# Performance work log

Measured on AMD Instinct MI355X. Metric: run time of the kernel, lower is better.

## Reference

```python
import jax, jax.numpy as jnp
import numpy as np

M1, M2 = 20, 20  # retained DCT modes per layer

def dct1_last(x):
    # scipy.fftpack unnormalized DCT-I along last axis via FFT of even extension
    N = x.shape[-1]
    ext = jnp.concatenate([x, x[..., -2:0:-1]], axis=-1)  # length 2N-2
    return jnp.fft.rfft(ext).real[..., :N]

def dct1_2d(x):
    x = dct1_last(x)                       # along axis -1
    x = dct1_last(x.swapaxes(-1, -2)).swapaxes(-1, -2)  # along axis -2
    return x

def setup_inputs() -> dict:
    key = jax.random.key(0)
    ks = jax.random.split(key, 11)
    B, X, Y, Din, C, FC, Dout, L = 8, 256, 256, 3, 64, 128, 1, 3
    scale = 1.0 / (C * C)
    return {
        "x": jax.random.normal(ks[0], (B, X, Y, Din), jnp.float32),
        "fc0_w": jax.random.normal(ks[1], (Din, C), jnp.float32) * 0.1,
        "fc0_b": jax.random.normal(ks[2], (C,), jnp.float32) * 0.1,
        "sp_w1": scale * jax.random.uniform(ks[3], (L, C, C, M1, M2), jnp.float32),
        "sp_w2": scale * jax.random.uniform(ks[4], (L, C, C, M1, M2), jnp.float32),
        "conv_w": jax.random.normal(ks[5], (L, C, C), jnp.float32) * 0.05,
        "conv_b": jax.random.normal(ks[6], (L, C), jnp.float32) * 0.05,
        "fc1_w": jax.random.normal(ks[7], (C, FC), jnp.float32) * 0.05,
        "fc1_b": jax.random.normal(ks[8], (FC,), jnp.float32) * 0.05,
        "fc2_w": jax.random.normal(ks[9], (FC, Dout), jnp.float32) * 0.05,
        "fc2_b": jax.random.normal(ks[10], (Dout,), jnp.float32) * 0.05,
    }

def reference(x, fc0_w, fc0_b, sp_w1, sp_w2, conv_w, conv_b, fc1_w, fc1_b, fc2_w, fc2_b):
    h = x @ fc0_w + fc0_b                  # (B, X, Y, C)
    h = h.transpose(0, 3, 1, 2)            # (B, C, X, Y)
    B, C, X, Y = h.shape
    n_layers = sp_w1.shape[0]
    for i in range(n_layers):
        hd = dct1_2d(h)                    # forward DCT-I (unnormalized)
        # spectral mode multiply, scattered into zero spectrum (imag part is 0)
        out = jnp.zeros((B, C, X, Y), h.dtype)
        out = out.at[:, :, :M1, :M2].set(
            jnp.einsum('bixy,ioxy->boxy', hd[:, :, :M1, :M2], sp_w1[i]))
        out = out.at[:, :, X - M1:, :M2].set(
            jnp.einsum('bixy,ioxy->boxy', hd[:, :, X - M1:, :M2], sp_w2[i]))
        x1 = dct1_2d(out)                  # fftpack idct type-1 == dct type-1 (unnormalized)
        x2 = jnp.einsum('bixy,oi->boxy', h, conv_w[i]) + conv_b[i][None, :, None, None]
        h = x1 + x2
        if i != n_layers - 1:
            h = jnp.tanh(h)
    h = h.transpose(0, 2, 3, 1)            # (B, X, Y, C)
    h = jnp.tanh(h @ fc1_w + fc1_b)
    return h @ fc2_w + fc2_b               # (B, X, Y, 1)
```

## Files before the change

### kernel.cpp

```cpp
#include <hip/hip_runtime.h>
#include <math.h>

#define BB    8
#define CC    64
#define NN    256
#define MM    20
#define NKK   40
#define NLAY  3
#define FCD   128
#define PLANE (NN*NN)

__device__ __forceinline__ float fast_tanh(float x) {
    float xc = fminf(fmaxf(x, -15.f), 15.f);
    float e = __expf(2.f * xc);
    return (e - 1.f) / (e + 1.f);
}

__global__ __launch_bounds__(256) void k_basis(float* __restrict__ FlT, float* __restrict__ FkT,
                                               float* __restrict__ BkT, float* __restrict__ BlT,
                                               float* __restrict__ CwT, const float* __restrict__ conv_w) {
    int t = threadIdx.x;
    const double PI = 3.14159265358979323846;
    for (int j = t; j < NN*MM; j += 256) {
        int y = j / MM, l = j % MM;
        double g = (y == 0 || y == NN-1) ? 1.0 : 2.0;
        FlT[j] = (float)(g * cos(PI * (double)(l*y) / (double)(NN-1)));
    }
    for (int j = t; j < NN*NKK; j += 256) {
        int x = j / NKK, k = j % NKK;
        int rk = (k < MM) ? k : (NN - NKK + k);
        double g = (x == 0 || x == NN-1) ? 1.0 : 2.0;
        FkT[j] = (float)(g * cos(PI * (double)(rk*x) / (double)(NN-1)));
    }
    for (int j = t; j < NKK*NN; j += 256) {
        int k = j / NN, p = j % NN;
        int rk = (k < MM) ? k : (NN - NKK + k);
        double g = (rk == 0 || rk == NN-1) ? 1.0 : 2.0;
        BkT[j] = (float)(g * cos(PI * (double)(rk*p) / (double)(NN-1)));
    }
    for (int j = t; j < MM*NN; j += 256) {
        int l = j / NN, q = j % NN;
        double g = (l == 0) ? 1.0 : 2.0;
        BlT[j] = (float)(g * cos(PI * (double)(q*l) / (double)(NN-1)));
    }
    for (int j = t; j < NLAY*CC*CC; j += 256) {
        int lay = j / (CC*CC), r = j % (CC*CC);
        int i = r / CC, o = r % CC;
        CwT[j] = conv_w[lay*CC*CC + o*CC + i];
    }
}

__global__ __launch_bounds__(256) void k_fc0(const float* __restrict__ xin, const float* __restrict__ w,
                                             const float* __restrict__ bias, float* __restrict__ h) {
    __shared__ float xs[NN*3];
    int b = blockIdx.x >> 8, p = blockIdx.x & 255, q = threadIdx.x;
    size_t rowbase = ((size_t)(b*NN + p)*NN) * 3;
    for (int j = q; j < NN*3; j += 256) xs[j] = xin[rowbase + j];
    __syncthreads();
    float v0 = xs[q*3+0], v1 = xs[q*3+1], v2 = xs[q*3+2];
    size_t obase = (size_t)b*CC*PLANE + (size_t)p*NN + q;
    #pragma unroll 8
    for (int c = 0; c < CC; ++c) {
        float hv = bias[c] + v0*w[c] + v1*w[CC+c] + v2*w[2*CC+c];
        h[obase + (size_t)c*PLANE] = hv;
    }
}

__global__ __launch_bounds__(256, 2) void k_fwd(const float* __restrict__ h, const float* __restrict__ FkT,
                                                const float* __restrict__ FlT, float* __restrict__ Gt) {
    __shared__ float P[NKK][NN+1];
    int plane = blockIdx.x;
    int t = threadIdx.x;
    const float* hp = h + (size_t)plane * PLANE;
    float acc[NKK];
    #pragma unroll 40
    for (int k = 0; k < NKK; ++k) acc[k] = 0.f;
    #pragma unroll 2
    for (int x = 0; x < NN; ++x) {
        float hv = hp[x*NN + t];
        const float* fr = &FkT[x*NKK];
        #pragma unroll 40
        for (int k = 0; k < NKK; ++k) acc[k] += fr[k] * hv;
    }
    #pragma unroll 40
    for (int k = 0; k < NKK; ++k) P[k][t] = acc[k];
    __syncthreads();
    int b = plane >> 6, c = plane & 63;
    for (int j = t; j < NKK*MM; j += 256) {
        int k = j / MM, l = j % MM;
        float a = 0.f;
        for (int y = 0; y < NN; ++y) a += P[k][y] * FlT[y*MM + l];
        Gt[((size_t)(k*BB + b)*CC + c)*MM + l] = a;
    }
}

__global__ __launch_bounds__(256, 2) void k_spec(const float* __restrict__ Gt, const float* __restrict__ w1,
                                                 const float* __restrict__ w2, float* __restrict__ S) {
    extern __shared__ float gl[];
    int kb = blockIdx.x;
    int t = threadIdx.x;
    const float* chunk = Gt + (size_t)kb * (BB*CC*MM);
    for (int j = t; j < BB*CC*MM; j += 256) gl[j] = chunk[j];
    __syncthreads();
    int o = t & 63, g = t >> 6;
    int b0 = 2*g, b1 = 2*g + 1;
    const float* wp; int kk;
    if (kb < MM) { wp = w1; kk = kb; } else { wp = w2; kk = kb - MM; }
    float a0[MM], a1[MM];
    #pragma unroll 20
    for (int l = 0; l < MM; ++l) { a0[l] = 0.f; a1[l] = 0.f; }
    for (int i = 0; i < CC; ++i) {
        const float4* wr4 = reinterpret_cast<const float4*>(wp + ((size_t)(i*CC + o)*MM + kk)*MM);
        const float4* g04 = reinterpret_cast<const float4*>(&gl[(b0*CC + i)*MM]);
        const float4* g14 = reinterpret_cast<const float4*>(&gl[(b1*CC + i)*MM]);
        #pragma unroll 5
        for (int l4 = 0; l4 < MM/4; ++l4) {
            float4 wv = wr4[l4];
            float4 gv0 = g04[l4];
            float4 gv1 = g14[l4];
            a0[4*l4+0] += wv.x*gv0.x; a0[4*l4+1] += wv.y*gv0.y;
            a0[4*l4+2] += wv.z*gv0.z; a0[4*l4+3] += wv.w*gv0.w;
            a1[4*l4+0] += wv.x*gv1.x; a1[4*l4+1] += wv.y*gv1.y;
            a1[4*l4+2] += wv.z*gv1.z; a1[4*l4+3] += wv.w*gv1.w;
        }
    }
    #pragma unroll 20
    for (int l = 0; l < MM; ++l) {
        S[((size_t)(b0*NKK + kb)*MM + l)*CC + o] = a0[l];
        S[((size_t)(b1*NKK + kb)*MM + l)*CC + o] = a1[l];
    }
}

__global__ __launch_bounds__(256, 2) void k_inv1(const float* __restrict__ S, const float* __restrict__ BkT,
                                                 float* __restrict__ U) {
    int b = blockIdx.x >> 8, p = blockIdx.x & 255;
    int o = threadIdx.x & 63, w = threadIdx.x >> 6;
    float acc[5];
    #pragma unroll 5
    for (int j = 0; j < 5; ++j) acc[j] = 0.f;
    for (int k = 0; k < NKK; ++k) {
        float bk = BkT[k*NN + p];
        const float* sb = S + ((size_t)(b*NKK + k)*MM + w)*CC + o;
        #pragma unroll 5
        for (int j = 0; j < 5; ++j) acc[j] += bk * sb[(size_t)(4*j)*CC];
    }
    float* ub = U + ((size_t)(b*NN + p)*MM + w)*CC + o;
    #pragma unroll 5
    for (int j = 0; j < 5; ++j) ub[(size_t)(4*j)*CC] = acc[j];
}

__global__ __launch_bounds__(256, 2) void k_combine(float* h, const float* __restrict__ U,
                                                    const float* __restrict__ BlT, const float* __restrict__ cwt,
                                                    const float* __restrict__ cb) {
    int b = blockIdx.x >> 8, p = blockIdx.x & 255;
    int q = threadIdx.x;
    float acc[CC];
    #pragma unroll 64
    for (int o = 0; o < CC; ++o) acc[o] = cb[o];
    float* hb = h + (size_t)b*CC*PLANE + (size_t)p*NN + q;
    #pragma unroll 4
    for (int i = 0; i < CC; ++i) {
        float hv = hb[(size_t)i*PLANE];
        const float* wr = &cwt[i*CC];
        #pragma unroll 64
        for (int o = 0; o < CC; ++o) acc[o] += wr[o]*hv;
    }
    const float* ub = U + ((size_t)(b*NN + p)*MM)*CC;
    #pragma unroll 2
    for (int l = 0; l < MM; ++l) {
        float blv = BlT[l*NN + q];
        const float* ur = ub + (size_t)l*CC;
        #pragma unroll 64
        for (int o = 0; o < CC; ++o) acc[o] += ur[o]*blv;
    }
    #pragma unroll 64
    for (int o = 0; o < CC; ++o) hb[(size_t)o*PLANE] = fast_tanh(acc[o]);
}

__global__ __launch_bounds__(256, 2) void k_combine_fc(const float* __restrict__ h, const float* __restrict__ U,
        const float* __restrict__ BlT, const float* __restrict__ cwt, const float* __restrict__ cb,
        const float* __restrict__ w1, const float* __restrict__ b1,
        const float* __restrict__ w2, const float* __restrict__ b2, float* __restrict__ out) {
    int b = blockIdx.x >> 8, p = blockIdx.x & 255;
    int q = threadIdx.x;
    float acc[CC];
    #pragma unroll 64
    for (int o = 0; o < CC; ++o) acc[o] = cb[o];
    const float* hb = h + (size_t)b*CC*PLANE + (size_t)p*NN + q;
    #pragma unroll 4
    for (int i = 0; i < CC; ++i) {
        float hv = hb[(size_t)i*PLANE];
        const float* wr = &cwt[i*CC];
        #pragma unroll 64
        for (int o = 0; o < CC; ++o) acc[o] += wr[o]*hv;
    }
    const float* ub = U + ((size_t)(b*NN + p)*MM)*CC;
    #pragma unroll 2
    for (int l = 0; l < MM; ++l) {
        float blv = BlT[l*NN + q];
        const float* ur = ub + (size_t)l*CC;
        #pragma unroll 64
        for (int o = 0; o < CC; ++o) acc[o] += ur[o]*blv;
    }
    float ov = b2[0];
    const int FCH = 8;
    for (int f0 = 0; f0 < FCD; f0 += FCH) {
        float a[FCH];
        #pragma unroll 8
        for (int f = 0; f < FCH; ++f) a[f] = b1[f0 + f];
        #pragma unroll 64
        for (int i = 0; i < CC; ++i) {
            float hv = acc[i];
            const float* wr = &w1[i*FCD + f0];
            #pragma unroll 8
            for (int f = 0; f < FCH; ++f) a[f] += hv*wr[f];
        }
        #pragma unroll 8
        for (int f = 0; f < FCH; ++f) ov += fast_tanh(a[f]) * w2[f0 + f];
    }
    out[(size_t)blockIdx.x*NN + q] = ov;
}

extern "C" void kernel_launch(void* const* d_in, const int* in_sizes, int n_in,
                              void* d_out, int out_size, void* d_ws, size_t ws_size,
                              hipStream_t stream) {
    const float* x      = (const float*)d_in[0];
    const float* fc0_w  = (const float*)d_in[1];
    const float* fc0_b  = (const float*)d_in[2];
    const float* sp_w1  = (const float*)d_in[3];
    const float* sp_w2  = (const float*)d_in[4];
    const float* conv_w = (const float*)d_in[5];
    const float* conv_b = (const float*)d_in[6];
    const float* fc1_w  = (const float*)d_in[7];
    const float* fc1_b  = (const float*)d_in[8];
    const float* fc2_w  = (const float*)d_in[9];
    const float* fc2_b  = (const float*)d_in[10];

    float* ws = (float*)d_ws;
    const size_t HSZ = (size_t)BB*CC*PLANE;
    float* hA  = ws;
    float* Gt  = hA + HSZ;
    float* S   = Gt + (size_t)NKK*BB*CC*MM;
    float* U   = S  + (size_t)BB*NKK*MM*CC;
    float* FlT = U  + (size_t)BB*NN*MM*CC;
    float* FkT = FlT + NN*MM;
    float* BkT = FkT + NN*NKK;
    float* BlT = BkT + NKK*NN;
    float* CwT = BlT + MM*NN;

    k_basis<<<1, 256, 0, stream>>>(FlT, FkT, BkT, BlT, CwT, conv_w);
    k_fc0<<<BB*NN, 256, 0, stream>>>(x, fc0_w, fc0_b, hA);

    for (int lay = 0; lay < NLAY; ++lay) {
        const float* w1 = sp_w1 + (size_t)lay*CC*CC*MM*MM;
        const float* w2 = sp_w2 + (size_t)lay*CC*CC*MM*MM;
        k_fwd<<<BB*CC, 256, 0, stream>>>(hA, FkT, FlT, Gt);
        k_spec<<<NKK, 256, BB*CC*MM*sizeof(float), stream>>>(Gt, w1, w2, S);
        k_inv1<<<BB*NN, 256, 0, stream>>>(S, BkT, U);
        if (lay != NLAY-1) {
            k_combine<<<BB*NN, 256, 0, stream>>>(
                hA, U, BlT, CwT + lay*CC*CC, conv_b + lay*CC);
        } else {
            k_combine_fc<<<BB*NN, 256, 0, stream>>>(
                hA, U, BlT, CwT + lay*CC*CC, conv_b + lay*CC,
                fc1_w, fc1_b, fc2_w, fc2_b, (float*)d_out);
        }
    }
}
```

Baseline: 1.060 ms.

## Split combine kernels across output-channel groups per wavefront to cut register pressure

Each combine block now covers 64 spatial columns, and its four wavefronts each own 16 output channels instead of one thread owning all 64 channels. This lowers per-thread accumulators from 64 to 16 to raise occupancy, at the price of four times as many blocks and each h element being loaded by four wavefronts. The in-place combine adds a __syncthreads before writing, so every wavefront has read h before any wavefront overwrites it. The final-layer kernel stages the 64-channel activation in shared memory, splits the FC1 hidden units across wavefronts, and reduces the partial outputs through shared memory.

```diff
diff --git a/kernel.cpp b/kernel.cpp
--- a/kernel.cpp
+++ b/kernel.cpp
@@ -152,73 +152,97 @@
 __global__ __launch_bounds__(256, 2) void k_combine(float* h, const float* __restrict__ U,
                                                     const float* __restrict__ BlT, const float* __restrict__ cwt,
                                                     const float* __restrict__ cb) {
-    int b = blockIdx.x >> 8, p = blockIdx.x & 255;
-    int q = threadIdx.x;
-    float acc[CC];
-    #pragma unroll 64
-    for (int o = 0; o < CC; ++o) acc[o] = cb[o];
+    int b = blockIdx.x >> 10, rem = blockIdx.x & 1023;
+    int p = rem >> 2, qc = rem & 3;
+    int lane = threadIdx.x & 63, w = threadIdx.x >> 6;
+    int q = qc*64 + lane, ob = w*16;
+    float acc[16];
+    {
+        const float* cbw = &cb[ob];
+        #pragma unroll 16
+        for (int o = 0; o < 16; ++o) acc[o] = cbw[o];
+    }
     float* hb = h + (size_t)b*CC*PLANE + (size_t)p*NN + q;
     #pragma unroll 4
     for (int i = 0; i < CC; ++i) {
         float hv = hb[(size_t)i*PLANE];
-        const float* wr = &cwt[i*CC];
-        #pragma unroll 64
-        for (int o = 0; o < CC; ++o) acc[o] += wr[o]*hv;
-    }
-    const float* ub = U + ((size_t)(b*NN + p)*MM)*CC;
-    #pragma unroll 2
+        const float* wr = &cwt[i*CC + ob];
+        #pragma unroll 16
+        for (int o = 0; o < 16; ++o) acc[o] += wr[o]*hv;
+    }
+    const float* ub = U + ((size_t)(b*NN + p)*MM)*CC + ob;
+    #pragma unroll 4
     for (int l = 0; l < MM; ++l) {
         float blv = BlT[l*NN + q];
         const float* ur = ub + (size_t)l*CC;
-        #pragma unroll 64
-        for (int o = 0; o < CC; ++o) acc[o] += ur[o]*blv;
-    }
-    #pragma unroll 64
-    for (int o = 0; o < CC; ++o) hb[(size_t)o*PLANE] = fast_tanh(acc[o]);
+        #pragma unroll 16
+        for (int o = 0; o < 16; ++o) acc[o] += ur[o]*blv;
+    }
+    __syncthreads();
+    #pragma unroll 16
+    for (int o = 0; o < 16; ++o) hb[(size_t)(ob + o)*PLANE] = fast_tanh(acc[o]);
 }
 
 __global__ __launch_bounds__(256, 2) void k_combine_fc(const float* __restrict__ h, const float* __restrict__ U,
         const float* __restrict__ BlT, const float* __restrict__ cwt, const float* __restrict__ cb,
         const float* __restrict__ w1, const float* __restrict__ b1,
         const float* __restrict__ w2, const float* __restrict__ b2, float* __restrict__ out) {
-    int b = blockIdx.x >> 8, p = blockIdx.x & 255;
-    int q = threadIdx.x;
-    float acc[CC];
-    #pragma unroll 64
-    for (int o = 0; o < CC; ++o) acc[o] = cb[o];
+    __shared__ float tile[CC][65];
+    __shared__ float part[4][64];
+    int b = blockIdx.x >> 10, rem = blockIdx.x & 1023;
+    int p = rem >> 2, qc = rem & 3;
+    int lane = threadIdx.x & 63, w = threadIdx.x >> 6;
+    int q = qc*64 + lane, ob = w*16;
+    float acc[16];
+    {
+        const float* cbw = &cb[ob];
+        #pragma unroll 16
+        for (int o = 0; o < 16; ++o) acc[o] = cbw[o];
+    }
     const float* hb = h + (size_t)b*CC*PLANE + (size_t)p*NN + q;
     #pragma unroll 4
     for (int i = 0; i < CC; ++i) {
         float hv = hb[(size_t)i*PLANE];
-        const float* wr = &cwt[i*CC];
-        #pragma unroll 64
-        for (int o = 0; o < CC; ++o) acc[o] += wr[o]*hv;
-    }
-    const float* ub = U + ((size_t)(b*NN + p)*MM)*CC;
-    #pragma unroll 2
+        const float* wr = &cwt[i*CC + ob];
+        #pragma unroll 16
+        for (int o = 0; o < 16; ++o) acc[o] += wr[o]*hv;
+    }
+    const float* ub = U + ((size_t)(b*NN + p)*MM)*CC + ob;
+    #pragma unroll 4
     for (int l = 0; l < MM; ++l) {
         float blv = BlT[l*NN + q];
         const float* ur = ub + (size_t)l*CC;
-        #pragma unroll 64
-        for (int o = 0; o < CC; ++o) acc[o] += ur[o]*blv;
-    }
-    float ov = b2[0];
-    const int FCH = 8;
-    for (int f0 = 0; f0 < FCD; f0 += FCH) {
-        float a[FCH];
-        #pragma unroll 8
-        for (int f = 0; f < FCH; ++f) a[f] = b1[f0 + f];
-        #pragma unroll 64
-        for (int i = 0; i < CC; ++i) {
-            float hv = acc[i];
-            const float* wr = &w1[i*FCD + f0];
-            #pragma unroll 8
-            for (int f = 0; f < FCH; ++f) a[f] += hv*wr[f];
-        }
-        #pragma unroll 8
-        for (int f = 0; f < FCH; ++f) ov += fast_tanh(a[f]) * w2[f0 + f];
-    }
-    out[(size_t)blockIdx.x*NN + q] = ov;
+        #pragma unroll 16
+        for (int o = 0; o < 16; ++o) acc[o] += ur[o]*blv;
+    }
+    #pragma unroll 16
+    for (int o = 0; o < 16; ++o) tile[ob + o][lane] = acc[o];
+    __syncthreads();
+    float a[32];
+    {
+        const float* bw = &b1[w*32];
+        #pragma unroll 32
+        for (int f = 0; f < 32; ++f) a[f] = bw[f];
+    }
+    #pragma unroll 2
+    for (int i = 0; i < CC; ++i) {
+        float hv = tile[i][lane];
+        const float* wr = &w1[i*FCD + w*32];
+        #pragma unroll 32
+        for (int f = 0; f < 32; ++f) a[f] += hv*wr[f];
+    }
+    float ov = 0.f;
+    {
+        const float* w2w = &w2[w*32];
+        #pragma unroll 32
+        for (int f = 0; f < 32; ++f) ov += fast_tanh(a[f]) * w2w[f];
+    }
+    part[w][lane] = ov;
+    __syncthreads();
+    if (threadIdx.x < 64) {
+        float r = b2[0] + part[0][lane] + part[1][lane] + part[2][lane] + part[3][lane];
+        out[((size_t)(b*NN + p)*NN) + qc*64 + lane] = r;
+    }
 }
 
 extern "C" void kernel_launch(void* const* d_in, const int* in_sizes, int n_in,
@@ -258,10 +282,10 @@
         k_spec<<<NKK, 256, BB*CC*MM*sizeof(float), stream>>>(Gt, w1, w2, S);
         k_inv1<<<BB*NN, 256, 0, stream>>>(S, BkT, U);
         if (lay != NLAY-1) {
-            k_combine<<<BB*NN, 256, 0, stream>>>(
+            k_combine<<<BB*NN*4, 256, 0, stream>>>(
                 hA, U, BlT, CwT + lay*CC*CC, conv_b + lay*CC);
         } else {
-            k_combine_fc<<<BB*NN, 256, 0, stream>>>(
+            k_combine_fc<<<BB*NN*4, 256, 0, stream>>>(
                 hA, U, BlT, CwT + lay*CC*CC, conv_b + lay*CC,
                 fc1_w, fc1_b, fc2_w, fc2_b, (float*)d_out);
         }
```

New measurement: 2.095 ms. 1.98x slower.

## Stage h column in LDS and compute combine outputs in 8-channel chunks

Applied to the files above, without the earlier changes.

The combine kernels now load the 64-channel input column into a 64KB shared tile and loop over output channels in groups of 8, instead of holding 64 accumulators in registers. The final kernel also writes the pre-activation back to global memory and reloads it into the tile for the FC layers. The aim is to cut register pressure and spilling. In exchange it adds 64KB of LDS per block, which caps occupancy, plus extra global round-trips and eight passes over the weights.

```diff
diff --git a/kernel.cpp b/kernel.cpp
--- a/kernel.cpp
+++ b/kernel.cpp
@@ -152,71 +152,96 @@
 __global__ __launch_bounds__(256, 2) void k_combine(float* h, const float* __restrict__ U,
                                                     const float* __restrict__ BlT, const float* __restrict__ cwt,
                                                     const float* __restrict__ cb) {
+    __shared__ float tile[CC][NN];
     int b = blockIdx.x >> 8, p = blockIdx.x & 255;
     int q = threadIdx.x;
-    float acc[CC];
-    #pragma unroll 64
-    for (int o = 0; o < CC; ++o) acc[o] = cb[o];
     float* hb = h + (size_t)b*CC*PLANE + (size_t)p*NN + q;
-    #pragma unroll 4
-    for (int i = 0; i < CC; ++i) {
-        float hv = hb[(size_t)i*PLANE];
-        const float* wr = &cwt[i*CC];
-        #pragma unroll 64
-        for (int o = 0; o < CC; ++o) acc[o] += wr[o]*hv;
-    }
+    #pragma unroll 8
+    for (int i = 0; i < CC; ++i) tile[i][q] = hb[(size_t)i*PLANE];
+    float blv[MM];
+    #pragma unroll 20
+    for (int l = 0; l < MM; ++l) blv[l] = BlT[l*NN + q];
     const float* ub = U + ((size_t)(b*NN + p)*MM)*CC;
-    #pragma unroll 2
-    for (int l = 0; l < MM; ++l) {
-        float blv = BlT[l*NN + q];
-        const float* ur = ub + (size_t)l*CC;
-        #pragma unroll 64
-        for (int o = 0; o < CC; ++o) acc[o] += ur[o]*blv;
-    }
-    #pragma unroll 64
-    for (int o = 0; o < CC; ++o) hb[(size_t)o*PLANE] = fast_tanh(acc[o]);
-}
-
-__global__ __launch_bounds__(256, 2) void k_combine_fc(const float* __restrict__ h, const float* __restrict__ U,
+    __syncthreads();
+    for (int oc = 0; oc < CC/8; ++oc) {
+        float acc8[8];
+        const float* cbw = &cb[oc*8];
+        #pragma unroll 8
+        for (int f = 0; f < 8; ++f) acc8[f] = cbw[f];
+        #pragma unroll 4
+        for (int i = 0; i < CC; ++i) {
+            float hv = tile[i][q];
+            const float* wr = &cwt[i*CC + oc*8];
+            #pragma unroll 8
+            for (int f = 0; f < 8; ++f) acc8[f] += wr[f]*hv;
+        }
+        #pragma unroll 4
+        for (int l = 0; l < MM; ++l) {
+            const float* ur = ub + (size_t)l*CC + oc*8;
+            #pragma unroll 8
+            for (int f = 0; f < 8; ++f) acc8[f] += ur[f]*blv[l];
+        }
+        #pragma unroll 8
+        for (int f = 0; f < 8; ++f) hb[(size_t)(oc*8+f)*PLANE] = fast_tanh(acc8[f]);
+    }
+}
+
+__global__ __launch_bounds__(256, 2) void k_combine_fc(float* h, const float* __restrict__ U,
         const float* __restrict__ BlT, const float* __restrict__ cwt, const float* __restrict__ cb,
         const float* __restrict__ w1, const float* __restrict__ b1,
         const float* __restrict__ w2, const float* __restrict__ b2, float* __restrict__ out) {
+    __shared__ float tile[CC][NN];
     int b = blockIdx.x >> 8, p = blockIdx.x & 255;
     int q = threadIdx.x;
-    float acc[CC];
-    #pragma unroll 64
-    for (int o = 0; o < CC; ++o) acc[o] = cb[o];
-    const float* hb = h + (size_t)b*CC*PLANE + (size_t)p*NN + q;
-    #pragma unroll 4
-    for (int i = 0; i < CC; ++i) {
-        float hv = hb[(size_t)i*PLANE];
-        const float* wr = &cwt[i*CC];
-        #pragma unroll 64
-        for (int o = 0; o < CC; ++o) acc[o] += wr[o]*hv;
-    }
+    float* hb = h + (size_t)b*CC*PLANE + (size_t)p*NN + q;
+    #pragma unroll 8
+    for (int i = 0; i < CC; ++i) tile[i][q] = hb[(size_t)i*PLANE];
+    float blv[MM];
+    #pragma unroll 20
+    for (int l = 0; l < MM; ++l) blv[l] = BlT[l*NN + q];
     const float* ub = U + ((size_t)(b*NN + p)*MM)*CC;
-    #pragma unroll 2
-    for (int l = 0; l < MM; ++l) {
-        float blv = BlT[l*NN + q];
-        const float* ur = ub + (size_t)l*CC;
-        #pragma unroll 64
-        for (int o = 0; o < CC; ++o) acc[o] += ur[o]*blv;
-    }
+    __syncthreads();
+    for (int oc = 0; oc < CC/8; ++oc) {
+        float acc8[8];
+        const float* cbw = &cb[oc*8];
+        #pragma unroll 8
+        for (int f = 0; f < 8; ++f) acc8[f] = cbw[f];
+        #pragma unroll 4
+        for (int i = 0; i < CC; ++i) {
+            float hv = tile[i][q];
+            const float* wr = &cwt[i*CC + oc*8];
+            #pragma unroll 8
+            for (int f = 0; f < 8; ++f) acc8[f] += wr[f]*hv;
+        }
+        #pragma unroll 4
+        for (int l = 0; l < MM; ++l) {
+            const float* ur = ub + (size_t)l*CC + oc*8;
+            #pragma unroll 8
+            for (int f = 0; f < 8; ++f) acc8[f] += ur[f]*blv[l];
+        }
+        #pragma unroll 8
+        for (int f = 0; f < 8; ++f) hb[(size_t)(oc*8+f)*PLANE] = acc8[f];
+    }
+    __syncthreads();
+    #pragma unroll 8
+    for (int i = 0; i < CC; ++i) tile[i][q] = hb[(size_t)i*PLANE];
+    __syncthreads();
     float ov = b2[0];
-    const int FCH = 8;
-    for (int f0 = 0; f0 < FCD; f0 += FCH) {
-        float a[FCH];
-        #pragma unroll 8
-        for (int f = 0; f < FCH; ++f) a[f] = b1[f0 + f];
-        #pragma unroll 64
+    for (int fc = 0; fc < FCD/8; ++fc) {
+        float a8[8];
+        const float* bw = &b1[fc*8];
+        #pragma unroll 8
+        for (int f = 0; f < 8; ++f) a8[f] = bw[f];
+        #pragma unroll 4
         for (int i = 0; i < CC; ++i) {
-            float hv = acc[i];
-            const float* wr = &w1[i*FCD + f0];
-            #pragma unroll 8
-            for (int f = 0; f < FCH; ++f) a[f] += hv*wr[f];
-        }
-        #pragma unroll 8
-        for (int f = 0; f < FCH; ++f) ov += fast_tanh(a[f]) * w2[f0 + f];
+            float hv = tile[i][q];
+            const float* wr = &w1[i*FCD + fc*8];
+            #pragma unroll 8
+            for (int f = 0; f < 8; ++f) a8[f] += hv*wr[f];
+        }
+        const float* w2w = &w2[fc*8];
+        #pragma unroll 8
+        for (int f = 0; f < 8; ++f) ov += fast_tanh(a8[f]) * w2w[f];
     }
     out[(size_t)blockIdx.x*NN + q] = ov;
 }
```

Result: slower. 1.379 ms (+30.1%).
